# Kernel tuning notes

Hardware: AMD Instinct MI355X
Metric: run time of the kernel (lower is better)

Reference implementation:

```python
import jax, jax.numpy as jnp
import numpy as np

B, N, DEG = 8, 4096, 16
E = N * DEG            # edges per graph
IN, HID, C, OUT = 128, 512, 2, 10
EPS = 1e-15


def setup_inputs() -> dict:
    key = jax.random.key(0)
    ks = jax.random.split(key, 16)
    # within-graph random edges, then offset each graph by b*N
    src = jax.random.randint(ks[0], (B, E), 0, N)
    dst = jax.random.randint(ks[1], (B, E), 0, N)
    off = (jnp.arange(B) * N)[:, None]
    edge_index = jnp.stack([(src + off).reshape(-1), (dst + off).reshape(-1)], axis=0).astype(jnp.int64)
    batch = jnp.repeat(jnp.arange(B), N).astype(jnp.int64)
    x = jax.random.normal(ks[2], (B * N, IN), dtype=jnp.float32)
    edge_weight = jax.random.uniform(ks[3], (B * E,), dtype=jnp.float32)
    g = lambda k, s: (0.02 * jax.random.normal(k, s, dtype=jnp.float32))
    return {
        "x": x, "edge_index": edge_index, "batch": batch, "edge_weight": edge_weight,
        "W_rel1": g(ks[4], (IN, HID)), "b_rel1": jnp.zeros((HID,), jnp.float32),
        "W_root1": g(ks[5], (IN, HID)),
        "W_pool": g(ks[6], (HID, C)), "b_pool": jnp.zeros((C,), jnp.float32),
        "W_rel3": g(ks[7], (HID, HID)), "b_rel3": jnp.zeros((HID,), jnp.float32),
        "W_root3": g(ks[8], (HID, HID)),
        "W_lin1": g(ks[9], (HID, HID)), "b_lin1": jnp.zeros((HID,), jnp.float32),
        "W_lin2": g(ks[10], (HID, OUT)), "b_lin2": jnp.zeros((OUT,), jnp.float32),
    }


def reference(x, edge_index, batch, edge_weight,
              W_rel1, b_rel1, W_root1, W_pool, b_pool,
              W_rel3, b_rel3, W_root3, W_lin1, b_lin1, W_lin2, b_lin2):
    src, dst = edge_index[0], edge_index[1]
    # GraphConv (aggr='add'): out = lin_rel(sum_j w_ji x_j) + lin_root(x)
    agg = jax.ops.segment_sum(x[src] * edge_weight[:, None], dst, num_segments=B * N)
    h = jax.nn.relu(agg @ W_rel1 + b_rel1 + x @ W_root1)          # [BN, HID]
    s_logits = h @ W_pool + b_pool                                 # [BN, C]

    # dense batched tensors (equal-size graphs)
    hd = h.reshape(B, N, HID)
    s = jax.nn.softmax(s_logits.reshape(B, N, C), axis=-1)
    b_idx = batch[src]
    r = src - b_idx * N
    c = dst - b_idx * N
    adj = jnp.zeros((B, N, N), jnp.float32).at[b_idx, r, c].add(edge_weight)

    # dense mincut pooling
    out = jnp.einsum('bnc,bnf->bcf', s, hd)                        # [B, C, HID]
    sA = jnp.einsum('bnc,bnm->bcm', s, adj)
    out_adj = jnp.einsum('bcm,bmk->bck', sA, s)                    # [B, C, C]
    mincut_num = jnp.einsum('bcc->b', out_adj)
    d = adj.sum(-1)                                                # [B, N]
    mincut_den = jnp.einsum('bnc,bn,bnc->b', s, d, s)
    mc_loss = jnp.mean(-(mincut_num / mincut_den))
    ss = jnp.einsum('bnc,bnk->bck', s, s)
    ss_n = ss / jnp.linalg.norm(ss, axis=(1, 2), keepdims=True)
    i_s = jnp.eye(C, dtype=jnp.float32) / jnp.sqrt(jnp.float32(C))
    o_loss = jnp.mean(jnp.linalg.norm(ss_n - i_s[None], axis=(1, 2)))
    # zero diagonal + symmetric degree normalization
    out_adj = out_adj * (1.0 - jnp.eye(C, dtype=jnp.float32))[None]
    d2 = jnp.sqrt(out_adj.sum(-1)) + EPS                           # [B, C]
    out_adj = out_adj / d2[:, :, None] / d2[:, None, :]

    # conv3 on pooled graph: edges (row->col) of dense adj => agg = A^T x
    agg3 = jnp.einsum('bij,bif->bjf', out_adj, out)
    x3 = agg3 @ W_rel3 + b_rel3 + out @ W_root3                    # [B, C, HID]
    xm = x3.mean(axis=1)                                           # [B, HID]
    h2 = jax.nn.relu(xm @ W_lin1 + b_lin1)
    logits = h2 @ W_lin2 + b_lin2
    return (jax.nn.log_softmax(logits, axis=-1), mc_loss, o_loss, s_logits, out_adj)
```

## Files before the change

### kernel.cpp

```cpp
#include <hip/hip_runtime.h>
#include <hip/hip_bf16.h>

#define BB 8
#define NN 4096
#define EE 65536
#define BE (BB*EE)
#define BN (BB*NN)
#define INF 128
#define HID 512
#define CC 2
#define OUTC 10
#define ELLCAP 64

typedef __bf16 bf16x8_t __attribute__((ext_vector_type(8)));
typedef float  f32x4_t  __attribute__((ext_vector_type(4)));

__device__ __forceinline__ ushort f2bf(float f) {
  union { float f; unsigned u; } v; v.f = f;
  unsigned r = v.u + 0x7FFFu + ((v.u >> 16) & 1u);
  return (ushort)(r >> 16);
}
__device__ __forceinline__ float bf2f(ushort s) {
  union { unsigned u; float f; } v; v.u = ((unsigned)s) << 16;
  return v.f;
}

__global__ __launch_bounds__(256) void front(
    const int* __restrict__ src, const int* __restrict__ dst,
    const float* __restrict__ ew, const float* __restrict__ x,
    const float* __restrict__ Wrel, const float* __restrict__ Wroot,
    int* __restrict__ deg, int2* __restrict__ ell,
    ushort* __restrict__ Ab, ushort* __restrict__ Bb) {
  int blk = blockIdx.x;
  int tid = threadIdx.x;
  if (blk < 4096) {
    int g = (blk & 7) * 131072 + (blk >> 3) * 256 + tid;
    float4 v = *(const float4*)&x[(size_t)g * 4];
    int m = g >> 5;
    int kin = (g & 31) * 4;
    ushort4 o;
    o.x = f2bf(v.x); o.y = f2bf(v.y); o.z = f2bf(v.z); o.w = f2bf(v.w);
    *(ushort4*)&Ab[(size_t)m * 256 + 128 + kin] = o;
  } else if (blk < 6144) {
    int bl = blk - 4096;
    int e = (bl & 7) * EE + (bl >> 3) * 256 + tid;
    int d = dst[e];
    int p = atomicAdd(&deg[d], 1);
    if (p < ELLCAP) {
      int2 v; v.x = src[e]; v.y = __float_as_int(ew[e]);
      ell[(size_t)d * ELLCAP + p] = v;
    }
  } else {
    int g = (blk - 6144) * 256 + tid;
    int n = g & 511, k = g >> 9;
    float w = (k < 128) ? Wrel[k * 512 + n] : Wroot[(k - 128) * 512 + n];
    Bb[n * 256 + k] = f2bf(w);
  }
}

__global__ __launch_bounds__(256) void gather_ell(
    const int* __restrict__ deg, const int2* __restrict__ ell,
    ushort* __restrict__ Ab) {
  int blk = blockIdx.x;
  int n = (blk & 7) * NN + (blk >> 3) * 4 + (threadIdx.x >> 6);
  int lane = threadIdx.x & 63;
  int l4 = lane >> 4;
  int fl = lane & 15;
  int d = deg[n]; if (d > ELLCAP) d = ELLCAP;
  const int2* ep = ell + (size_t)n * ELLCAP;

  float a[8] = {0, 0, 0, 0, 0, 0, 0, 0};
  int j = 0;
  for (; j + 7 < d; j += 8) {
    int2 v0 = ep[j + l4];
    int2 v1 = ep[j + 4 + l4];
    uint4 u0 = *(const uint4*)&Ab[(size_t)v0.x * 256 + 128 + fl * 8];
    uint4 u1 = *(const uint4*)&Ab[(size_t)v1.x * 256 + 128 + fl * 8];
    float w0 = __int_as_float(v0.y);
    float w1 = __int_as_float(v1.y);
    const ushort* s0 = (const ushort*)&u0;
    const ushort* s1 = (const ushort*)&u1;
#pragma unroll
    for (int q = 0; q < 8; ++q)
      a[q] += w0 * bf2f(s0[q]) + w1 * bf2f(s1[q]);
  }
  for (; j + 3 < d; j += 4) {
    int2 v0 = ep[j + l4];
    uint4 u0 = *(const uint4*)&Ab[(size_t)v0.x * 256 + 128 + fl * 8];
    float w0 = __int_as_float(v0.y);
    const ushort* s0 = (const ushort*)&u0;
#pragma unroll
    for (int q = 0; q < 8; ++q)
      a[q] += w0 * bf2f(s0[q]);
  }
  {
    int idx = j + l4;
    if (idx < d) {
      int2 v0 = ep[idx];
      uint4 u0 = *(const uint4*)&Ab[(size_t)v0.x * 256 + 128 + fl * 8];
      float w0 = __int_as_float(v0.y);
      const ushort* s0 = (const ushort*)&u0;
#pragma unroll
      for (int q = 0; q < 8; ++q)
        a[q] += w0 * bf2f(s0[q]);
    }
  }
#pragma unroll
  for (int q = 0; q < 8; ++q) {
    a[q] += __shfl_xor(a[q], 16, 64);
    a[q] += __shfl_xor(a[q], 32, 64);
  }
  if (l4 == 0) {
    ushort o[8];
#pragma unroll
    for (int q = 0; q < 8; ++q) o[q] = f2bf(a[q]);
    *(uint4*)&Ab[(size_t)n * 256 + fl * 8] = *(const uint4*)o;
  }
}

#define CPAD 72
__global__ __launch_bounds__(256) void gemm_mfma(
    const ushort* __restrict__ Ab, const ushort* __restrict__ Bb,
    const float* __restrict__ brel, ushort* __restrict__ hw) {
  __shared__ ushort As[64 * 256];
  __shared__ ushort Bs[64 * 256];
  int tid = threadIdx.x;
  int blk = blockIdx.x;
  int xcd = blk & 7;
  int idx = blk >> 3;
  int by = xcd * 64 + (idx & 63);
  int bx = idx >> 6;
  int m0 = by * 64, n0 = bx * 64;

#pragma unroll
  for (int i = 0; i < 8; ++i) {
    int g = tid + i * 256;
    int r = g >> 5, c = g & 31;
    int cs = c ^ (r & 31);
    *(uint4*)&As[(r * 32 + cs) * 8] = *(const uint4*)&Ab[(size_t)(m0 + r) * 256 + c * 8];
    *(uint4*)&Bs[(r * 32 + cs) * 8] = *(const uint4*)&Bb[(size_t)(n0 + r) * 256 + c * 8];
  }
  __syncthreads();

  int wave = tid >> 6, lane = tid & 63;
  int wm = (wave >> 1) * 32, wn = (wave & 1) * 32;
  int l16 = lane & 15, quad = lane >> 4;

  f32x4_t acc[2][2];
#pragma unroll
  for (int f = 0; f < 2; ++f)
#pragma unroll
    for (int g = 0; g < 2; ++g) acc[f][g] = (f32x4_t){0.f, 0.f, 0.f, 0.f};

  int arow[2] = {wm + l16, wm + 16 + l16};
  int brow[2] = {wn + l16, wn + 16 + l16};

#pragma unroll
  for (int kc = 0; kc < 8; ++kc) {
    int cl = kc * 4 + quad;
    bf16x8_t af[2], bf[2];
#pragma unroll
    for (int f = 0; f < 2; ++f) {
      af[f] = *(const bf16x8_t*)&As[(arow[f] * 32 + (cl ^ (arow[f] & 31))) * 8];
      bf[f] = *(const bf16x8_t*)&Bs[(brow[f] * 32 + (cl ^ (brow[f] & 31))) * 8];
    }
#pragma unroll
    for (int f = 0; f < 2; ++f)
#pragma unroll
      for (int g = 0; g < 2; ++g)
        acc[f][g] = __builtin_amdgcn_mfma_f32_16x16x32_bf16(af[f], bf[g], acc[f][g], 0, 0, 0);
  }
  __syncthreads();

  ushort* Cs = As;
#pragma unroll
  for (int g = 0; g < 2; ++g) {
    int col = wn + g * 16 + l16;
    float bias = brel[n0 + col];
#pragma unroll
    for (int f = 0; f < 2; ++f) {
      int rowb = wm + f * 16 + quad * 4;
#pragma unroll
      for (int r = 0; r < 4; ++r) {
        float v = fmaxf(acc[f][g][r] + bias, 0.f);
        Cs[(rowb + r) * CPAD + col] = f2bf(v);
      }
    }
  }
  __syncthreads();
  {
    int r = tid >> 2, co = (tid & 3) * 16;
    uint4 v0 = *(uint4*)&Cs[r * CPAD + co];
    uint4 v1 = *(uint4*)&Cs[r * CPAD + co + 8];
    *(uint4*)&hw[(size_t)(m0 + r) * 512 + n0 + co] = v0;
    *(uint4*)&hw[(size_t)(m0 + r) * 512 + n0 + co + 8] = v1;
  }
}

__global__ __launch_bounds__(256) void pool_node(
    const ushort* __restrict__ hw, const float* __restrict__ Wp,
    const float* __restrict__ bp, float* __restrict__ s,
    float* __restrict__ slog, float* __restrict__ outpart,
    float* __restrict__ ssacc) {
  __shared__ float red[4][1024];
  __shared__ float ssr[4][3];
  int blk = blockIdx.x;
  int b = blk & 7;
  int chunk = blk >> 3;
  int obik = b * 64 + chunk;
  int wave = threadIdx.x >> 6, lane = threadIdx.x & 63;
  int n0 = b * NN + chunk * 64 + wave * 16;
  int f0 = lane * 8;

  float wp0[8], wp1[8];
#pragma unroll
  for (int j = 0; j < 8; ++j) {
    wp0[j] = Wp[(f0 + j) * 2];
    wp1[j] = Wp[(f0 + j) * 2 + 1];
  }
  float bp0 = bp[0], bp1 = bp[1];
  float o0[8] = {0, 0, 0, 0, 0, 0, 0, 0};
  float o1[8] = {0, 0, 0, 0, 0, 0, 0, 0};
  float sa = 0.f, sb = 0.f, sc2 = 0.f;

  for (int i = 0; i < 16; ++i) {
    int n = n0 + i;
    bf16x8_t hv = *(const bf16x8_t*)&hw[(size_t)n * HID + f0];
    const ushort* hp = (const ushort*)&hv;
    float h[8];
    float a0 = 0.f, a1 = 0.f;
#pragma unroll
    for (int j = 0; j < 8; ++j) {
      h[j] = bf2f(hp[j]);
      a0 += h[j] * wp0[j];
      a1 += h[j] * wp1[j];
    }
#pragma unroll
    for (int off = 32; off; off >>= 1) {
      a0 += __shfl_down(a0, off, 64);
      a1 += __shfl_down(a1, off, 64);
    }
    float s0 = 0.f, s1 = 0.f;
    if (lane == 0) {
      float l0 = a0 + bp0, l1 = a1 + bp1;
      slog[n * 2] = l0;
      slog[n * 2 + 1] = l1;
      float m = fmaxf(l0, l1);
      float e0 = expf(l0 - m), e1 = expf(l1 - m);
      float inv = 1.f / (e0 + e1);
      s0 = e0 * inv; s1 = e1 * inv;
      s[n * 2] = s0;
      s[n * 2 + 1] = s1;
      sa += s0 * s0; sb += s0 * s1; sc2 += s1 * s1;
    }
    s0 = __shfl(s0, 0, 64);
    s1 = __shfl(s1, 0, 64);
#pragma unroll
    for (int j = 0; j < 8; ++j) {
      o0[j] += s0 * h[j];
      o1[j] += s1 * h[j];
    }
  }

#pragma unroll
  for (int j = 0; j < 8; ++j) {
    red[wave][f0 + j] = o0[j];
    red[wave][512 + f0 + j] = o1[j];
  }
  if (lane == 0) { ssr[wave][0] = sa; ssr[wave][1] = sb; ssr[wave][2] = sc2; }
  __syncthreads();
  int t = threadIdx.x;
#pragma unroll
  for (int q = 0; q < 4; ++q) {
    int idx = t + q * 256;
    float v = red[0][idx] + red[1][idx] + red[2][idx] + red[3][idx];
    outpart[(size_t)obik * 1024 + idx] = v;
  }
  if (t < 3) {
    float v = ssr[0][t] + ssr[1][t] + ssr[2][t] + ssr[3][t];
    atomicAdd(&ssacc[b * 4 + t], v);
  }
}

__global__ __launch_bounds__(256) void edge_pass2(
    const int* __restrict__ src, const int* __restrict__ dst,
    const float* __restrict__ ew, const float* __restrict__ s,
    float* __restrict__ oadj, float* __restrict__ mden) {
  int b = blockIdx.x & 7;
  int sub = blockIdx.x >> 3;
  int base = b * EE + sub * 1024;
  float p00 = 0, p01 = 0, p10 = 0, p11 = 0, md = 0;
  for (int i = threadIdx.x; i < 1024; i += 256) {
    int e = base + i;
    int r = src[e], c = dst[e];
    float w = ew[e];
    float s0r = s[r * 2], s1r = s[r * 2 + 1];
    float s0c = s[c * 2], s1c = s[c * 2 + 1];
    p00 += w * s0r * s0c; p01 += w * s0r * s1c;
    p10 += w * s1r * s0c; p11 += w * s1r * s1c;
    md  += w * (s0r * s0r + s1r * s1r);
  }
#pragma unroll
  for (int off = 32; off; off >>= 1) {
    p00 += __shfl_down(p00, off, 64);
    p01 += __shfl_down(p01, off, 64);
    p10 += __shfl_down(p10, off, 64);
    p11 += __shfl_down(p11, off, 64);
    md  += __shfl_down(md,  off, 64);
  }
  __shared__ float red[4][5];
  int wave = threadIdx.x >> 6, lane = threadIdx.x & 63;
  if (lane == 0) {
    red[wave][0] = p00; red[wave][1] = p01;
    red[wave][2] = p10; red[wave][3] = p11;
    red[wave][4] = md;
  }
  __syncthreads();
  if (threadIdx.x < 4) {
    float v = red[0][threadIdx.x] + red[1][threadIdx.x] +
              red[2][threadIdx.x] + red[3][threadIdx.x];
    atomicAdd(&oadj[b * 4 + threadIdx.x], v);
  } else if (threadIdx.x == 4) {
    float v = red[0][4] + red[1][4] + red[2][4] + red[3][4];
    atomicAdd(&mden[b], v);
  }
}

__global__ __launch_bounds__(256) void finalize_a(
    const float* __restrict__ outpart, const float* __restrict__ oadj,
    const float* __restrict__ ssacc, const float* __restrict__ mden,
    float* __restrict__ uv, float* __restrict__ dout) {
  __shared__ float sc[2];
  int b = blockIdx.x, t = threadIdx.x;
  if (t == 0) {
    float r00 = oadj[b * 4 + 0], r01 = oadj[b * 4 + 1];
    float r10 = oadj[b * 4 + 2], r11 = oadj[b * 4 + 3];
    atomicAdd(&dout[80], -((r00 + r11) / mden[b]) / (float)BB);
    float a = ssacc[b * 4 + 0], bb = ssacc[b * 4 + 1], c = ssacc[b * 4 + 2];
    float nrm = sqrtf(a * a + 2.f * bb * bb + c * c);
    float q = 0.70710678118654752f;
    float da = a / nrm - q, db = bb / nrm, dc = c / nrm - q;
    atomicAdd(&dout[81], sqrtf(da * da + 2.f * db * db + dc * dc) / (float)BB);
    float d20 = sqrtf(r01) + 1e-15f;
    float d21 = sqrtf(r10) + 1e-15f;
    float oa01 = r01 / (d20 * d21);
    float oa10 = r10 / (d21 * d20);
    dout[65618 + b * 4 + 0] = 0.f;
    dout[65618 + b * 4 + 1] = oa01;
    dout[65618 + b * 4 + 2] = oa10;
    dout[65618 + b * 4 + 3] = 0.f;
    sc[0] = oa01; sc[1] = oa10;
  }
  __syncthreads();
  float oa01 = sc[0], oa10 = sc[1];
  for (int f = t; f < HID; f += 256) {
    float o0 = 0.f, o1 = 0.f;
    for (int i = 0; i < 64; ++i) {
      o0 += outpart[(size_t)(b * 64 + i) * 1024 + f];
      o1 += outpart[(size_t)(b * 64 + i) * 1024 + 512 + f];
    }
    uv[b * HID + f] = oa10 * o1 + oa01 * o0;
    uv[BB * HID + b * HID + f] = o0 + o1;
  }
}

__global__ __launch_bounds__(256) void conv3_part(
    const float* __restrict__ uv, const float* __restrict__ Wrel3,
    const float* __restrict__ Wroot3, float* __restrict__ xmacc) {
  __shared__ float us[8][32], vs[8][32];
  __shared__ float red[4][64][8];
  int blk = blockIdx.x;
  int fc = blk & 7, kc = blk >> 3;
  int t = threadIdx.x;
  {
    int b = t >> 5, k = t & 31;
    us[b][k] = uv[b * HID + kc * 32 + k];
    vs[b][k] = uv[BB * HID + b * HID + kc * 32 + k];
  }
  __syncthreads();
  int f = fc * 64 + (t & 63);
  int ks = t >> 6;
  float acc[8] = {0, 0, 0, 0, 0, 0, 0, 0};
#pragma unroll
  for (int j = 0; j < 8; ++j) {
    int kl = ks * 8 + j;
    int k = kc * 32 + kl;
    float wr = Wrel3[k * HID + f];
    float wo = Wroot3[k * HID + f];
#pragma unroll
    for (int b = 0; b < 8; ++b)
      acc[b] += us[b][kl] * wr + vs[b][kl] * wo;
  }
#pragma unroll
  for (int b = 0; b < 8; ++b) red[ks][t & 63][b] = acc[b];
  __syncthreads();
  if (ks == 0) {
    int fl = t & 63;
#pragma unroll
    for (int b = 0; b < 8; ++b) {
      float v = red[0][fl][b] + red[1][fl][b] + red[2][fl][b] + red[3][fl][b];
      atomicAdd(&xmacc[b * HID + f], v);
    }
  }
}

__global__ __launch_bounds__(256) void lin1_part(
    const float* __restrict__ xmacc, const float* __restrict__ brel3,
    const float* __restrict__ Wlin1, float* __restrict__ h2acc) {
  __shared__ float xs[8][32];
  __shared__ float red[4][64][8];
  int blk = blockIdx.x;
  int fc = blk & 7, kc = blk >> 3;
  int t = threadIdx.x;
  {
    int b = t >> 5, k = t & 31;
    xs[b][k] = 0.5f * xmacc[b * HID + kc * 32 + k] + brel3[kc * 32 + k];
  }
  __syncthreads();
  int f = fc * 64 + (t & 63);
  int ks = t >> 6;
  float acc[8] = {0, 0, 0, 0, 0, 0, 0, 0};
#pragma unroll
  for (int j = 0; j < 8; ++j) {
    int kl = ks * 8 + j;
    int k = kc * 32 + kl;
    float w = Wlin1[k * HID + f];
#pragma unroll
    for (int b = 0; b < 8; ++b)
      acc[b] += xs[b][kl] * w;
  }
#pragma unroll
  for (int b = 0; b < 8; ++b) red[ks][t & 63][b] = acc[b];
  __syncthreads();
  if (ks == 0) {
    int fl = t & 63;
#pragma unroll
    for (int b = 0; b < 8; ++b) {
      float v = red[0][fl][b] + red[1][fl][b] + red[2][fl][b] + red[3][fl][b];
      atomicAdd(&h2acc[b * HID + f], v);
    }
  }
}

__global__ __launch_bounds__(256) void head(
    const float* __restrict__ h2acc, const float* __restrict__ blin1,
    const float* __restrict__ Wlin2, const float* __restrict__ blin2,
    float* __restrict__ dout) {
  __shared__ float hs[HID];
  __shared__ float lg[16];
  __shared__ float lse;
  int b = blockIdx.x, t = threadIdx.x;
  for (int i = t; i < HID; i += 256)
    hs[i] = fmaxf(h2acc[b * HID + i] + blin1[i], 0.f);
  __syncthreads();
  int wave = t >> 6, lane = t & 63;
  for (int o = wave; o < OUTC; o += 4) {
    float acc = 0.f;
    for (int k = lane; k < HID; k += 64)
      acc += hs[k] * Wlin2[k * OUTC + o];
#pragma unroll
    for (int off = 32; off; off >>= 1) acc += __shfl_down(acc, off, 64);
    if (lane == 0) lg[o] = acc + blin2[o];
  }
  __syncthreads();
  if (t == 0) {
    float m = lg[0];
    for (int o = 1; o < OUTC; ++o) m = fmaxf(m, lg[o]);
    float se = 0.f;
    for (int o = 0; o < OUTC; ++o) se += expf(lg[o] - m);
    lse = m + logf(se);
  }
  __syncthreads();
  if (t < OUTC) dout[b * OUTC + t] = lg[t] - lse;
}

extern "C" void kernel_launch(void* const* d_in, const int* in_sizes, int n_in,
                              void* d_out, int out_size, void* d_ws, size_t ws_size,
                              hipStream_t stream) {
  const float* x      = (const float*)d_in[0];
  const int*   ei     = (const int*)d_in[1];
  const float* ew     = (const float*)d_in[3];
  const float* Wrel1  = (const float*)d_in[4];
  const float* brel1  = (const float*)d_in[5];
  const float* Wroot1 = (const float*)d_in[6];
  const float* Wpool  = (const float*)d_in[7];
  const float* bpool  = (const float*)d_in[8];
  const float* Wrel3  = (const float*)d_in[9];
  const float* brel3  = (const float*)d_in[10];
  const float* Wroot3 = (const float*)d_in[11];
  const float* Wlin1  = (const float*)d_in[12];
  const float* blin1  = (const float*)d_in[13];
  const float* Wlin2  = (const float*)d_in[14];
  const float* blin2  = (const float*)d_in[15];
  float* out = (float*)d_out;
  float* ws  = (float*)d_ws;

  float* oadj  = ws + 40960;
  float* ssacc = oadj + 32;
  float* mden  = ssacc + 32;
  int*   deg   = (int*)(mden + 8);
  float* xmacc = ws + 73800;
  float* h2acc = xmacc + 4096;
  ushort* Ab   = (ushort*)(ws + 106568);
  ushort* Bb   = (ushort*)(ws + 4300872);
  ushort* hbf  = (ushort*)(ws + 4366408);
  float* outpart = ws + 12763208;
  int2*  ell   = (int2*)(ws + 4366408);
  float* s     = ws + 106568;
  float* uv    = (float*)deg;

  const int* src = ei;
  const int* dst = ei + BE;

  hipMemsetAsync(ws + 40960, 0, (size_t)41032 * sizeof(float), stream);
  hipMemsetAsync(out + 80, 0, 2 * sizeof(float), stream);

  front      <<<6656, 256, 0, stream>>>(src, dst, ew, x, Wrel1, Wroot1,
                                        deg, ell, Ab, Bb);
  gather_ell <<<BN / 4, 256, 0, stream>>>(deg, ell, Ab);
  gemm_mfma  <<<4096, 256, 0, stream>>>(Ab, Bb, brel1, hbf);
  pool_node  <<<512, 256, 0, stream>>>(hbf, Wpool, bpool, s, out + 82, outpart, ssacc);
  edge_pass2 <<<BB * 64, 256, 0, stream>>>(src, dst, ew, s, oadj, mden);
  finalize_a <<<BB, 256, 0, stream>>>(outpart, oadj, ssacc, mden, uv, out);
  conv3_part <<<128, 256, 0, stream>>>(uv, Wrel3, Wroot3, xmacc);
  lin1_part  <<<128, 256, 0, stream>>>(xmacc, brel3, Wlin1, h2acc);
  head       <<<BB, 256, 0, stream>>>(h2acc, blin1, Wlin2, blin2, out);
}
```

Measured before the change: 218.0 us.

## Fold conv3 and lin1 weights into one precomputed matrix product in front kernel

Because there is no nonlinearity between conv3's mean and lin1, the code precomputes 0.5*W_rel3@W_lin1, 0.5*W_root3@W_lin1 and the folded bias inside the front kernel. The tail then needs a single fused kernel that reduces the pooled features, applies the folded weights, does the ReLU and Wlin2 partial logits, followed by a tiny log-softmax kernel. This cuts three serial tail launches and their atomic round trips. In exchange, the front kernel does a 512x512x512 weight product on every call (512 extra blocks with uncoalesced strided Wsrc reads), which may add more work than it saves.

```diff
diff --git a/kernel.cpp b/kernel.cpp
--- a/kernel.cpp
+++ b/kernel.cpp
@@ -29,8 +29,12 @@
     const int* __restrict__ src, const int* __restrict__ dst,
     const float* __restrict__ ew, const float* __restrict__ x,
     const float* __restrict__ Wrel, const float* __restrict__ Wroot,
+    const float* __restrict__ Wrel3, const float* __restrict__ Wroot3,
+    const float* __restrict__ brel3,
+    const float* __restrict__ Wlin1, const float* __restrict__ blin1,
     int* __restrict__ deg, int2* __restrict__ ell,
-    ushort* __restrict__ Ab, ushort* __restrict__ Bb) {
+    ushort* __restrict__ Ab, ushort* __restrict__ Bb,
+    float* __restrict__ Wa, float* __restrict__ Wb, float* __restrict__ bc) {
   int blk = blockIdx.x;
   int tid = threadIdx.x;
   if (blk < 4096) {
@@ -50,11 +54,46 @@
       int2 v; v.x = src[e]; v.y = __float_as_int(ew[e]);
       ell[(size_t)d * ELLCAP + p] = v;
     }
-  } else {
+  } else if (blk < 6656) {
     int g = (blk - 6144) * 256 + tid;
     int n = g & 511, k = g >> 9;
     float w = (k < 128) ? Wrel[k * 512 + n] : Wroot[(k - 128) * 512 + n];
     Bb[n * 256 + k] = f2bf(w);
+  } else if (blk < 7168) {
+    int p = blk - 6656;
+    int wsel = p & 1;
+    int q = p >> 1;
+    int fc = q & 7, kc = q >> 3;
+    const float* Wsrc = wsel ? Wroot3 : Wrel3;
+    float* Wdst = wsel ? Wb : Wa;
+    int f = fc * 64 + (tid & 63);
+    int k0 = kc * 16 + (tid >> 6) * 4;
+    float acc0 = 0.f, acc1 = 0.f, acc2 = 0.f, acc3 = 0.f;
+    for (int j = 0; j < 512; ++j) {
+      float wl = Wlin1[j * 512 + f];
+      acc0 += Wsrc[(k0 + 0) * 512 + j] * wl;
+      acc1 += Wsrc[(k0 + 1) * 512 + j] * wl;
+      acc2 += Wsrc[(k0 + 2) * 512 + j] * wl;
+      acc3 += Wsrc[(k0 + 3) * 512 + j] * wl;
+    }
+    Wdst[(k0 + 0) * 512 + f] = 0.5f * acc0;
+    Wdst[(k0 + 1) * 512 + f] = 0.5f * acc1;
+    Wdst[(k0 + 2) * 512 + f] = 0.5f * acc2;
+    Wdst[(k0 + 3) * 512 + f] = 0.5f * acc3;
+  } else {
+    __shared__ float red[4][64];
+    int bcb = blk - 7168;
+    int f = bcb * 64 + (tid & 63);
+    int ks = tid >> 6;
+    float acc = 0.f;
+    for (int j = ks * 128; j < ks * 128 + 128; ++j)
+      acc += brel3[j] * Wlin1[j * 512 + f];
+    red[ks][tid & 63] = acc;
+    __syncthreads();
+    if (ks == 0) {
+      float v = red[0][tid] + red[1][tid] + red[2][tid] + red[3][tid];
+      bc[f] = v + blin1[f];
+    }
   }
 }
 
@@ -326,142 +365,81 @@
   }
 }
 
-__global__ __launch_bounds__(256) void finalize_a(
+__global__ __launch_bounds__(256) void h2logits(
     const float* __restrict__ outpart, const float* __restrict__ oadj,
     const float* __restrict__ ssacc, const float* __restrict__ mden,
-    float* __restrict__ uv, float* __restrict__ dout) {
+    const float* __restrict__ Wa, const float* __restrict__ Wb,
+    const float* __restrict__ bcv, const float* __restrict__ Wlin2,
+    float* __restrict__ lacc, float* __restrict__ dout) {
+  __shared__ float oarr[1024];
+  __shared__ float red[4][64];
   __shared__ float sc[2];
-  int b = blockIdx.x, t = threadIdx.x;
+  int b = blockIdx.x >> 3, fc = blockIdx.x & 7;
+  int t = threadIdx.x;
   if (t == 0) {
     float r00 = oadj[b * 4 + 0], r01 = oadj[b * 4 + 1];
     float r10 = oadj[b * 4 + 2], r11 = oadj[b * 4 + 3];
-    atomicAdd(&dout[80], -((r00 + r11) / mden[b]) / (float)BB);
-    float a = ssacc[b * 4 + 0], bb = ssacc[b * 4 + 1], c = ssacc[b * 4 + 2];
-    float nrm = sqrtf(a * a + 2.f * bb * bb + c * c);
-    float q = 0.70710678118654752f;
-    float da = a / nrm - q, db = bb / nrm, dc = c / nrm - q;
-    atomicAdd(&dout[81], sqrtf(da * da + 2.f * db * db + dc * dc) / (float)BB);
     float d20 = sqrtf(r01) + 1e-15f;
     float d21 = sqrtf(r10) + 1e-15f;
     float oa01 = r01 / (d20 * d21);
     float oa10 = r10 / (d21 * d20);
-    dout[65618 + b * 4 + 0] = 0.f;
-    dout[65618 + b * 4 + 1] = oa01;
-    dout[65618 + b * 4 + 2] = oa10;
-    dout[65618 + b * 4 + 3] = 0.f;
     sc[0] = oa01; sc[1] = oa10;
+    if (fc == 0) {
+      atomicAdd(&dout[80], -((r00 + r11) / mden[b]) / (float)BB);
+      float a = ssacc[b * 4 + 0], bb = ssacc[b * 4 + 1], c = ssacc[b * 4 + 2];
+      float nrm = sqrtf(a * a + 2.f * bb * bb + c * c);
+      float q = 0.70710678118654752f;
+      float da = a / nrm - q, db = bb / nrm, dc = c / nrm - q;
+      atomicAdd(&dout[81], sqrtf(da * da + 2.f * db * db + dc * dc) / (float)BB);
+      dout[65618 + b * 4 + 0] = 0.f;
+      dout[65618 + b * 4 + 1] = oa01;
+      dout[65618 + b * 4 + 2] = oa10;
+      dout[65618 + b * 4 + 3] = 0.f;
+    }
+  }
+#pragma unroll
+  for (int q = 0; q < 4; ++q) {
+    int idx = t + q * 256;
+    float sacc = 0.f;
+    for (int i = 0; i < 64; ++i)
+      sacc += outpart[(size_t)(b * 64 + i) * 1024 + idx];
+    oarr[idx] = sacc;
   }
   __syncthreads();
   float oa01 = sc[0], oa10 = sc[1];
-  for (int f = t; f < HID; f += 256) {
-    float o0 = 0.f, o1 = 0.f;
-    for (int i = 0; i < 64; ++i) {
-      o0 += outpart[(size_t)(b * 64 + i) * 1024 + f];
-      o1 += outpart[(size_t)(b * 64 + i) * 1024 + 512 + f];
-    }
-    uv[b * HID + f] = oa10 * o1 + oa01 * o0;
-    uv[BB * HID + b * HID + f] = o0 + o1;
-  }
-}
-
-__global__ __launch_bounds__(256) void conv3_part(
-    const float* __restrict__ uv, const float* __restrict__ Wrel3,
-    const float* __restrict__ Wroot3, float* __restrict__ xmacc) {
-  __shared__ float us[8][32], vs[8][32];
-  __shared__ float red[4][64][8];
-  int blk = blockIdx.x;
-  int fc = blk & 7, kc = blk >> 3;
-  int t = threadIdx.x;
-  {
-    int b = t >> 5, k = t & 31;
-    us[b][k] = uv[b * HID + kc * 32 + k];
-    vs[b][k] = uv[BB * HID + b * HID + kc * 32 + k];
-  }
-  __syncthreads();
   int f = fc * 64 + (t & 63);
   int ks = t >> 6;
-  float acc[8] = {0, 0, 0, 0, 0, 0, 0, 0};
-#pragma unroll
-  for (int j = 0; j < 8; ++j) {
-    int kl = ks * 8 + j;
-    int k = kc * 32 + kl;
-    float wr = Wrel3[k * HID + f];
-    float wo = Wroot3[k * HID + f];
-#pragma unroll
-    for (int b = 0; b < 8; ++b)
-      acc[b] += us[b][kl] * wr + vs[b][kl] * wo;
-  }
-#pragma unroll
-  for (int b = 0; b < 8; ++b) red[ks][t & 63][b] = acc[b];
-  __syncthreads();
-  if (ks == 0) {
-    int fl = t & 63;
-#pragma unroll
-    for (int b = 0; b < 8; ++b) {
-      float v = red[0][fl][b] + red[1][fl][b] + red[2][fl][b] + red[3][fl][b];
-      atomicAdd(&xmacc[b * HID + f], v);
-    }
-  }
-}
-
-__global__ __launch_bounds__(256) void lin1_part(
-    const float* __restrict__ xmacc, const float* __restrict__ brel3,
-    const float* __restrict__ Wlin1, float* __restrict__ h2acc) {
-  __shared__ float xs[8][32];
-  __shared__ float red[4][64][8];
-  int blk = blockIdx.x;
-  int fc = blk & 7, kc = blk >> 3;
-  int t = threadIdx.x;
-  {
-    int b = t >> 5, k = t & 31;
-    xs[b][k] = 0.5f * xmacc[b * HID + kc * 32 + k] + brel3[kc * 32 + k];
-  }
-  __syncthreads();
-  int f = fc * 64 + (t & 63);
-  int ks = t >> 6;
-  float acc[8] = {0, 0, 0, 0, 0, 0, 0, 0};
-#pragma unroll
-  for (int j = 0; j < 8; ++j) {
-    int kl = ks * 8 + j;
-    int k = kc * 32 + kl;
-    float w = Wlin1[k * HID + f];
-#pragma unroll
-    for (int b = 0; b < 8; ++b)
-      acc[b] += xs[b][kl] * w;
-  }
-#pragma unroll
-  for (int b = 0; b < 8; ++b) red[ks][t & 63][b] = acc[b];
-  __syncthreads();
-  if (ks == 0) {
-    int fl = t & 63;
-#pragma unroll
-    for (int b = 0; b < 8; ++b) {
-      float v = red[0][fl][b] + red[1][fl][b] + red[2][fl][b] + red[3][fl][b];
-      atomicAdd(&h2acc[b * HID + f], v);
-    }
-  }
-}
-
-__global__ __launch_bounds__(256) void head(
-    const float* __restrict__ h2acc, const float* __restrict__ blin1,
-    const float* __restrict__ Wlin2, const float* __restrict__ blin2,
+  float acc = 0.f;
+  for (int kq = 0; kq < 128; ++kq) {
+    int k = ks * 128 + kq;
+    float o0 = oarr[k], o1 = oarr[512 + k];
+    float u = oa10 * o1 + oa01 * o0;
+    float v = o0 + o1;
+    acc += u * Wa[k * 512 + f] + v * Wb[k * 512 + f];
+  }
+  red[ks][t & 63] = acc;
+  __syncthreads();
+  if (t < 64) {
+    int ff = fc * 64 + t;
+    float h2 = red[0][t] + red[1][t] + red[2][t] + red[3][t] + bcv[ff];
+    h2 = fmaxf(h2, 0.f);
+#pragma unroll
+    for (int o = 0; o < OUTC; ++o) {
+      float lp = h2 * Wlin2[ff * OUTC + o];
+#pragma unroll
+      for (int off = 32; off; off >>= 1) lp += __shfl_down(lp, off, 64);
+      if (t == 0) atomicAdd(&lacc[b * 16 + o], lp);
+    }
+  }
+}
+
+__global__ __launch_bounds__(64) void headfinal(
+    const float* __restrict__ lacc, const float* __restrict__ blin2,
     float* __restrict__ dout) {
-  __shared__ float hs[HID];
   __shared__ float lg[16];
   __shared__ float lse;
   int b = blockIdx.x, t = threadIdx.x;
-  for (int i = t; i < HID; i += 256)
-    hs[i] = fmaxf(h2acc[b * HID + i] + blin1[i], 0.f);
-  __syncthreads();
-  int wave = t >> 6, lane = t & 63;
-  for (int o = wave; o < OUTC; o += 4) {
-    float acc = 0.f;
-    for (int k = lane; k < HID; k += 64)
-      acc += hs[k] * Wlin2[k * OUTC + o];
-#pragma unroll
-    for (int off = 32; off; off >>= 1) acc += __shfl_down(acc, off, 64);
-    if (lane == 0) lg[o] = acc + blin2[o];
-  }
+  if (t < OUTC) lg[t] = lacc[b * 16 + t] + blin2[t];
   __syncthreads();
   if (t == 0) {
     float m = lg[0];
@@ -499,30 +477,31 @@
   float* ssacc = oadj + 32;
   float* mden  = ssacc + 32;
   int*   deg   = (int*)(mden + 8);
-  float* xmacc = ws + 73800;
-  float* h2acc = xmacc + 4096;
+  float* lacc  = ws + 73800;
   ushort* Ab   = (ushort*)(ws + 106568);
   ushort* Bb   = (ushort*)(ws + 4300872);
   ushort* hbf  = (ushort*)(ws + 4366408);
   float* outpart = ws + 12763208;
+  float* Wa  = ws + 16000000;
+  float* Wb  = ws + 16262144;
+  float* bcv = ws + 16524288;
   int2*  ell   = (int2*)(ws + 4366408);
   float* s     = ws + 106568;
-  float* uv    = (float*)deg;
 
   const int* src = ei;
   const int* dst = ei + BE;
 
-  hipMemsetAsync(ws + 40960, 0, (size_t)41032 * sizeof(float), stream);
+  hipMemsetAsync(ws + 40960, 0, (size_t)32968 * sizeof(float), stream);
   hipMemsetAsync(out + 80, 0, 2 * sizeof(float), stream);
 
-  front      <<<6656, 256, 0, stream>>>(src, dst, ew, x, Wrel1, Wroot1,
-                                        deg, ell, Ab, Bb);
+  front      <<<7176, 256, 0, stream>>>(src, dst, ew, x, Wrel1, Wroot1,
+                                        Wrel3, Wroot3, brel3, Wlin1, blin1,
+                                        deg, ell, Ab, Bb, Wa, Wb, bcv);
   gather_ell <<<BN / 4, 256, 0, stream>>>(deg, ell, Ab);
   gemm_mfma  <<<4096, 256, 0, stream>>>(Ab, Bb, brel1, hbf);
   pool_node  <<<512, 256, 0, stream>>>(hbf, Wpool, bpool, s, out + 82, outpart, ssacc);
   edge_pass2 <<<BB * 64, 256, 0, stream>>>(src, dst, ew, s, oadj, mden);
-  finalize_a <<<BB, 256, 0, stream>>>(outpart, oadj, ssacc, mden, uv, out);
-  conv3_part <<<128, 256, 0, stream>>>(uv, Wrel3, Wroot3, xmacc);
-  lin1_part  <<<128, 256, 0, stream>>>(xmacc, brel3, Wlin1, h2acc);
-  head       <<<BB, 256, 0, stream>>>(h2acc, blin1, Wlin2, blin2, out);
-}
+  h2logits   <<<64, 256, 0, stream>>>(outpart, oadj, ssacc, mden,
+                                      Wa, Wb, bcv, Wlin2, lacc, out);
+  headfinal  <<<BB, 64, 0, stream>>>(lacc, blin2, out);
+}
```

Result: slower. 305.6 us (+40.2%).
